# Performance work log

Hardware: AMD Instinct MI355X
Metric: run time of the kernel (lower is better)

The kernel has to match this reference:

```python
import math
import jax, jax.numpy as jnp
import numpy as np

EPS_NORM = 1e-6
EPS_COS = 1e-6


def setup_inputs() -> dict:
    key = jax.random.key(0)
    ks = jax.random.split(key, 6)
    B, C, T, H, W = 2, 768, 8, 24, 24
    d_head = 64
    nh = C // d_head  # 12
    x = jax.random.normal(ks[0], (B, C, T, H, W), jnp.float32)
    pos = jax.random.uniform(ks[1], (B, H, W, 2), jnp.float32)
    cond = jax.random.normal(ks[2], (B, C), jnp.float32)
    # NOTE: original zero-inits norm.linear and out_proj; we use small random
    # weights so the reference exercises the full math path.
    norm_w = jax.random.normal(ks[3], (C, C), jnp.float32) * 0.02
    qkv_w = jax.random.normal(ks[4], (3 * C, C), jnp.float32) * (1.0 / math.sqrt(C))
    scale = jnp.full((nh,), 10.0, jnp.float32)
    out_w = jax.random.normal(ks[5], (C, C), jnp.float32) * 0.02
    # AxialRoPE freqs buffer, exactly as in torch:
    dim = d_head // 2
    n = nh * dim // 4
    lf = np.linspace(math.log(math.pi), math.log(10.0 * math.pi), n + 1)[:-1]
    freqs = jnp.asarray(np.exp(lf).reshape(dim // 4, nh).T, jnp.float32)  # [nh, d_head//8]
    return dict(x=x, pos=pos, cond=cond, norm_w=norm_w, qkv_w=qkv_w,
                scale=scale, out_w=out_w, freqs=freqs)


def reference(x, pos, cond, norm_w, qkv_w, scale, out_w, freqs):
    B, C, T, H, W = x.shape
    nh = freqs.shape[0]
    e = C // nh
    s = H * W
    n = B * T
    skip = x

    # b c t h w -> (b t) h w c
    xr = jnp.transpose(x, (0, 2, 3, 4, 1)).reshape(n, H, W, C)
    # cond: b c -> (b t) c
    condr = jnp.repeat(cond, T, axis=0)

    # AdaRMSNorm
    cs = condr @ norm_w.T + 1.0  # [n, C]
    ms = jnp.mean(xr.astype(jnp.float32) ** 2, axis=-1, keepdims=True)
    xn = (xr * (cs[:, None, None, :] * jax.lax.rsqrt(ms + EPS_NORM))).astype(x.dtype)

    # QKV projection
    qkv = xn @ qkv_w.T  # [n, H, W, 3C]
    qkv = qkv.reshape(n, s, 3, nh, e)
    q = jnp.transpose(qkv[:, :, 0], (0, 2, 1, 3))  # [n, nh, s, e]
    k = jnp.transpose(qkv[:, :, 1], (0, 2, 1, 3))
    v = jnp.transpose(qkv[:, :, 2], (0, 2, 1, 3))

    # cosine-sim QK rescale (per-head learned scale)
    sq = jnp.sqrt(scale)[:, None, None]  # [nh,1,1]
    q = q * (sq * jax.lax.rsqrt(jnp.sum(q ** 2, axis=-1, keepdims=True) + EPS_COS))
    k = k * (sq * jax.lax.rsqrt(jnp.sum(k ** 2, axis=-1, keepdims=True) + EPS_COS))

    # axial RoPE: theta [B, s, nh, 2*dth] -> repeat over T -> [n, nh, s, d]
    posf = pos.reshape(B, s, 2)
    th = posf[:, :, 0, None, None] * freqs  # [B, s, nh, dth]
    tw = posf[:, :, 1, None, None] * freqs
    theta = jnp.concatenate([th, tw], axis=-1)
    theta = jnp.repeat(theta, T, axis=0)
    theta = jnp.transpose(theta, (0, 2, 1, 3))  # [n, nh, s, d]
    cos_t, sin_t = jnp.cos(theta), jnp.sin(theta)
    d = theta.shape[-1]

    def rot(t):
        t1, t2, rest = t[..., :d], t[..., d:2 * d], t[..., 2 * d:]
        return jnp.concatenate([t1 * cos_t - t2 * sin_t,
                                t2 * cos_t + t1 * sin_t, rest], axis=-1)

    q = rot(q)
    k = rot(k)

    # SDPA with scale=1.0
    attn = jax.nn.softmax(jnp.einsum('bhqe,bhke->bhqk', q, k), axis=-1)
    o = jnp.einsum('bhqk,bhke->bhqe', attn, v)  # [n, nh, s, e]

    # n nh (h w) e -> n h w (nh e)
    o = jnp.transpose(o, (0, 2, 1, 3)).reshape(n, H, W, C)
    o = o @ out_w.T
    # (b t) h w c -> b c t h w
    o = o.reshape(B, T, H, W, C).transpose(0, 4, 1, 2, 3)
    return o + skip
```

## Files before the change

### kernel.cpp

```cpp
#include <hip/hip_runtime.h>
#include <hip/hip_bf16.h>

#define CDIM 768
#define NHEAD 12
#define EDIM 64
#define TDIM 8
#define SDIM 576
#define NROW 16
#define MDIM 9216
#define QKVN 2304

typedef __attribute__((ext_vector_type(4))) float f32x4;
typedef __bf16 bf16x8 __attribute__((ext_vector_type(8)));
typedef unsigned short u16;
typedef __attribute__((ext_vector_type(8))) unsigned short u16x8;

__device__ inline float bf2f(u16 u) {
  union { unsigned int i; float f; } x; x.i = ((unsigned int)u) << 16; return x.f;
}
__device__ inline u16 f2bf(float f) {
  union { float f; unsigned int i; } x; x.f = f;
  unsigned int i = x.i;
  return (u16)((i + 0x7FFFu + ((i >> 16) & 1u)) >> 16);
}
__device__ inline unsigned cvt_pk_bf16(float lo, float hi) {
  unsigned r;
  asm("v_cvt_pk_bf16_f32 %0, %1, %2" : "=v"(r) : "v"(lo), "v"(hi));
  return r;
}

__global__ __launch_bounds__(256) void cs_kernel(const float* __restrict__ cond,
                                                 const float* __restrict__ nw,
                                                 float* __restrict__ cs) {
  int idx = blockIdx.x * 256 + threadIdx.x;
  int b = idx / CDIM, c = idx % CDIM;
  const float* cr = cond + (size_t)b * CDIM;
  const float* wr = nw + (size_t)c * CDIM;
  float s = 1.0f;
  for (int j = 0; j < CDIM; j += 4) {
    float4 a = *(const float4*)(cr + j);
    float4 w = *(const float4*)(wr + j);
    s = fmaf(a.x, w.x, s); s = fmaf(a.y, w.y, s);
    s = fmaf(a.z, w.z, s); s = fmaf(a.w, w.w, s);
  }
  cs[idx] = s;
}

__global__ __launch_bounds__(256) void norm_kernel(const float* __restrict__ x,
                                                   const float* __restrict__ cs,
                                                   u16* __restrict__ xn) {
  __shared__ float xs[16][772];
  __shared__ float red[16][17];
  __shared__ float rfac[16];
  int n = blockIdx.y;
  int hw0 = blockIdx.x * 16;
  int b = n >> 3, t = n & 7;
  int tx = threadIdx.x, ty = threadIdx.y;
  const float* xb = x + ((size_t)b * CDIM * TDIM + t) * SDIM;
  float acc = 0.0f;
  for (int c = ty; c < CDIM; c += 16) {
    float v = xb[(size_t)c * (TDIM * SDIM) + hw0 + tx];
    xs[tx][c] = v;
    acc = fmaf(v, v, acc);
  }
  red[ty][tx] = acc;
  __syncthreads();
  if (ty == 0) {
    float s = 0.0f;
    #pragma unroll
    for (int j = 0; j < 16; j++) s += red[j][tx];
    rfac[tx] = rsqrtf(s * (1.0f / (float)CDIM) + 1e-6f);
  }
  __syncthreads();
  const float* csb = cs + (size_t)b * CDIM;
  int flat = ty * 16 + tx;
  #pragma unroll
  for (int i = 0; i < 6; i++) {
    int idx = i * 256 + flat;
    int row = idx / 96;
    int cseg = idx - row * 96;
    int c0 = cseg * 8;
    float rf = rfac[row];
    float4 a0 = *(const float4*)&xs[row][c0];
    float4 a1 = *(const float4*)&xs[row][c0 + 4];
    float4 w0 = *(const float4*)(csb + c0);
    float4 w1 = *(const float4*)(csb + c0 + 4);
    u16x8 ov;
    ov[0] = f2bf(a0.x * w0.x * rf); ov[1] = f2bf(a0.y * w0.y * rf);
    ov[2] = f2bf(a0.z * w0.z * rf); ov[3] = f2bf(a0.w * w0.w * rf);
    ov[4] = f2bf(a1.x * w1.x * rf); ov[5] = f2bf(a1.y * w1.y * rf);
    ov[6] = f2bf(a1.z * w1.z * rf); ov[7] = f2bf(a1.w * w1.w * rf);
    *(u16x8*)(xn + ((size_t)n * SDIM + hw0 + row) * CDIM + c0) = ov;
  }
}

__global__ __launch_bounds__(256) void convert_kernel(const float* __restrict__ src,
                                                      u16* __restrict__ dst, int count4) {
  int i = blockIdx.x * 256 + threadIdx.x;
  if (i < count4) {
    float4 v = *(const float4*)(src + (size_t)i * 4);
    u16* d = dst + (size_t)i * 4;
    d[0] = f2bf(v.x); d[1] = f2bf(v.y); d[2] = f2bf(v.z); d[3] = f2bf(v.w);
  }
}

__device__ __forceinline__ void gemm_bt_lds(const u16* __restrict__ A,
                                            const u16* __restrict__ B,
                                            int K, int m0, int n0, int tid,
                                            u16* ldsA, u16* ldsB,
                                            f32x4 acc[4][4]) {
  int lane = tid & 63;
  int wid = tid >> 6;
  int wm = (wid >> 1) * 64, wn = (wid & 1) * 64;
  int lr = lane & 15, lg = lane >> 4;
  const u16* gA = A + (size_t)(m0 + wid * 32 + (lane >> 3)) * K + (((lane & 7) ^ (lane >> 3)) * 8);
  const u16* gB = B + (size_t)(n0 + wid * 32 + (lane >> 3)) * K + (((lane & 7) ^ (lane >> 3)) * 8);
  u16* dA = ldsA + wid * 2048;
  u16* dB = ldsB + wid * 2048;
  auto STAGE = [&](int buf, int k0) {
    u16* dAb = dA + buf * 8192;
    u16* dBb = dB + buf * 8192;
    #pragma unroll
    for (int is = 0; is < 4; is++) {
      __builtin_amdgcn_global_load_lds(
          (const __attribute__((address_space(1))) unsigned int*)(gA + (size_t)(is * 8) * K + k0),
          (__attribute__((address_space(3))) unsigned int*)(dAb + is * 512),
          16, 0, 0);
      __builtin_amdgcn_global_load_lds(
          (const __attribute__((address_space(1))) unsigned int*)(gB + (size_t)(is * 8) * K + k0),
          (__attribute__((address_space(3))) unsigned int*)(dBb + is * 512),
          16, 0, 0);
    }
  };
  int nt = K >> 6;
  STAGE(0, 0);
  int cur = 0;
  #pragma unroll 1
  for (int t = 0; t < nt; t++) {
    if (t + 1 < nt) {
      STAGE(cur ^ 1, (t + 1) * 64);
      asm volatile("s_waitcnt vmcnt(8)" ::: "memory");
    } else {
      asm volatile("s_waitcnt vmcnt(0)" ::: "memory");
    }
    __builtin_amdgcn_s_barrier();
    __builtin_amdgcn_sched_barrier(0);
    const u16* lA = ldsA + cur * 8192;
    const u16* lB = ldsB + cur * 8192;
    #pragma unroll
    for (int kk = 0; kk < 2; kk++) {
      bf16x8 af[4], bfr[4];
      #pragma unroll
      for (int i = 0; i < 4; i++)
        af[i]  = *(const bf16x8*)&lA[(wm + i * 16 + lr) * 64 + (((lg + 4 * kk) ^ (lr & 7)) * 8)];
      #pragma unroll
      for (int j = 0; j < 4; j++)
        bfr[j] = *(const bf16x8*)&lB[(wn + j * 16 + lr) * 64 + (((lg + 4 * kk) ^ (lr & 7)) * 8)];
      #pragma unroll
      for (int i = 0; i < 4; i++)
        #pragma unroll
        for (int j = 0; j < 4; j++)
          acc[i][j] = __builtin_amdgcn_mfma_f32_16x16x32_bf16(af[i], bfr[j], acc[i][j], 0, 0, 0);
    }
    __builtin_amdgcn_sched_barrier(0);
    __builtin_amdgcn_s_barrier();
    __builtin_amdgcn_sched_barrier(0);
    cur ^= 1;
  }
}

__device__ __forceinline__ void swz_tile(int L, int& m0, int& n0) {
  int xcd = L & 7, loc = L >> 3;
  int nblk = loc / 9, mloc = loc - nblk * 9;
  m0 = (xcd * 9 + mloc) * 128;
  n0 = nblk * 128;
}

__global__ __launch_bounds__(256) void gemm_qkv(const u16* __restrict__ xn,
                                                const u16* __restrict__ wq,
                                                const float* __restrict__ pos,
                                                const float* __restrict__ freqs,
                                                const float* __restrict__ scale,
                                                u16* __restrict__ q,
                                                u16* __restrict__ k,
                                                u16* __restrict__ vt) {
  __shared__ u16 smem[32768];
  u16* ldsA = smem;
  u16* ldsB = smem + 16384;
  f32x4 acc[4][4] = {};
  int tid = threadIdx.x;
  int m0, n0;
  swz_tile(blockIdx.x, m0, n0);
  gemm_bt_lds(xn, wq, CDIM, m0, n0, tid, ldsA, ldsB, acc);
  int lane = tid & 63, wid = tid >> 6;
  int wm = (wid >> 1) * 64, wn = (wid & 1) * 64;
  int lr = lane & 15, rb = (lane >> 4) * 4;
  int part = n0 / CDIM;
  int hbase = (n0 - part * CDIM) >> 6;
  u16* T = smem;
  if (part < 2) {
    int h = hbase + (wn >> 6);
    float fr = freqs[h * 8 + (lr & 7)];
    float sq = sqrtf(scale[h]) * (part == 0 ? 1.44269504f : 1.0f);
    #pragma unroll
    for (int i = 0; i < 4; i++)
      #pragma unroll
      for (int r = 0; r < 4; r++) {
        int m = m0 + wm + i * 16 + rb + r;
        int nidx = m / SDIM, sp = m - nidx * SDIM;
        int b = nidx >> 3;
        float2 pp = *(const float2*)&pos[((size_t)b * SDIM + sp) * 2];
        float th = (lr < 8 ? pp.x : pp.y) * fr;
        float sth, cth;
        __sincosf(th, &sth, &cth);
        float v0 = acc[i][0][r];
        float v1 = acc[i][1][r];
        float v2 = acc[i][2][r];
        float v3 = acc[i][3][r];
        float ss = v0 * v0 + v1 * v1 + v2 * v2 + v3 * v3;
        ss += __shfl_xor(ss, 1); ss += __shfl_xor(ss, 2);
        ss += __shfl_xor(ss, 4); ss += __shfl_xor(ss, 8);
        float rs = sq * rsqrtf(ss + 1e-6f);
        v0 *= rs; v1 *= rs; v2 *= rs; v3 *= rs;
        float o0 = v0 * cth - v1 * sth;
        float o1 = v1 * cth + v0 * sth;
        u16* trow = T + (size_t)(wm + i * 16 + rb + r) * 136 + wn + lr;
        trow[0]  = f2bf(o0); trow[16] = f2bf(o1);
        trow[32] = f2bf(v2); trow[48] = f2bf(v3);
      }
    __syncthreads();
    u16* dst = (part == 0) ? q : k;
    #pragma unroll
    for (int c = 0; c < 8; c++) {
      int chunk = c * 256 + tid;
      int ml = chunk >> 4, sub = chunk & 15;
      int m = m0 + ml;
      int nidx = m / SDIM, sp = m - nidx * SDIM;
      int hl = sub >> 3, e0 = (sub & 7) * 8;
      u16x8 v = *(const u16x8*)&T[(size_t)ml * 136 + sub * 8];
      *(u16x8*)(dst + ((size_t)(nidx * NHEAD + hbase + hl) * SDIM + sp) * EDIM + e0) = v;
    }
  } else {
    #pragma unroll
    for (int i = 0; i < 4; i++)
      #pragma unroll
      for (int j = 0; j < 4; j++)
        #pragma unroll
        for (int r = 0; r < 4; r++)
          T[(size_t)(wn + j * 16 + lr) * 136 + (wm + i * 16 + rb + r)] = f2bf(acc[i][j][r]);
    __syncthreads();
    #pragma unroll
    for (int c = 0; c < 8; c++) {
      int chunk = c * 256 + tid;
      int nl = chunk >> 4, sub = chunk & 15;
      int hl = nl >> 6, e = nl & 63;
      int m = m0 + sub * 8;
      int nidx = m / SDIM, hw = m - nidx * SDIM;
      u16x8 v = *(const u16x8*)&T[(size_t)nl * 136 + sub * 8];
      *(u16x8*)(vt + ((size_t)(nidx * NHEAD + hbase + hl) * EDIM + e) * SDIM + hw) = v;
    }
  }
}

__global__ __launch_bounds__(256, 2) void attn_mfma(const u16* __restrict__ q,
                                                    const u16* __restrict__ k,
                                                    const u16* __restrict__ vt,
                                                    u16* __restrict__ o) {
  __shared__ u16 kbuf[2][4096];
  __shared__ u16 vbuf[2][4096];
  __shared__ u16 p_lds[4][48][72];
  int L = blockIdx.x;
  int cid = (L & 7) * 72 + (L >> 3);
  int nh_ = cid / 3;
  int qt = cid - nh_ * 3;
  int n = nh_ / NHEAD, h = nh_ - n * NHEAD;
  int tid = threadIdx.x;
  int wid = tid >> 6, lane = tid & 63;
  int lr = lane & 15, lg = lane >> 4;
  int qbase = qt * 192 + wid * 48;

  const u16* qp = q + ((size_t)nh_ * SDIM + qbase) * EDIM;
  bf16x8 qa[3][2];
  #pragma unroll
  for (int f = 0; f < 3; f++) {
    qa[f][0] = *(const bf16x8*)(qp + (size_t)(f * 16 + lr) * EDIM + lg * 8);
    qa[f][1] = *(const bf16x8*)(qp + (size_t)(f * 16 + lr) * EDIM + 32 + lg * 8);
  }
  const u16* kb = k + (size_t)nh_ * SDIM * EDIM;
  const u16* vb = vt + (size_t)nh_ * EDIM * SDIM;

  int srow = wid * 16 + (lane >> 3);
  int schunk = (lane & 7) ^ (lane >> 3);
  auto STAGE = [&](int buf, int s0) {
    #pragma unroll
    for (int is = 0; is < 2; is++) {
      int row = srow + is * 8;
      __builtin_amdgcn_global_load_lds(
          (const __attribute__((address_space(1))) unsigned int*)(kb + (size_t)(s0 + row) * EDIM + schunk * 8),
          (__attribute__((address_space(3))) unsigned int*)(&kbuf[buf][(size_t)(wid * 16 + is * 8 + (lane >> 3)) * 64 + (lane & 7) * 8]),
          16, 0, 0);
      __builtin_amdgcn_global_load_lds(
          (const __attribute__((address_space(1))) unsigned int*)(vb + (size_t)row * SDIM + s0 + schunk * 8),
          (__attribute__((address_space(3))) unsigned int*)(&vbuf[buf][(size_t)(wid * 16 + is * 8 + (lane >> 3)) * 64 + (lane & 7) * 8]),
          16, 0, 0);
    }
  };

  float psum[3] = {0.0f, 0.0f, 0.0f};
  f32x4 oacc[3][4] = {};

  STAGE(0, 0);
  int cur = 0;
  #pragma unroll 1
  for (int kt = 0; kt < 9; kt++) {
    if (kt < 8) {
      STAGE(cur ^ 1, (kt + 1) * 64);
      asm volatile("s_waitcnt vmcnt(4)" ::: "memory");
    } else {
      asm volatile("s_waitcnt vmcnt(0)" ::: "memory");
    }
    __builtin_amdgcn_s_barrier();
    __builtin_amdgcn_sched_barrier(0);
    const u16* kl = kbuf[cur];
    const u16* vl = vbuf[cur];
    bf16x8 kf[4][2];
    #pragma unroll
    for (int j = 0; j < 4; j++) {
      kf[j][0] = *(const bf16x8*)&kl[(j * 16 + lr) * 64 + ((lg       ^ (lr & 7)) * 8)];
      kf[j][1] = *(const bf16x8*)&kl[(j * 16 + lr) * 64 + (((lg + 4) ^ (lr & 7)) * 8)];
    }
    bf16x8 vf[2][4];
    #pragma unroll
    for (int ks = 0; ks < 2; ks++)
      #pragma unroll
      for (int et = 0; et < 4; et++)
        vf[ks][et] = *(const bf16x8*)&vl[(et * 16 + lr) * 64 + (((ks * 4 + lg) ^ (lr & 7)) * 8)];
    #pragma unroll
    for (int f = 0; f < 3; f++) {
      f32x4 sfr[4] = {};
      #pragma unroll
      for (int j = 0; j < 4; j++) {
        sfr[j] = __builtin_amdgcn_mfma_f32_16x16x32_bf16(kf[j][0], qa[f][0], sfr[j], 0, 0, 0);
        sfr[j] = __builtin_amdgcn_mfma_f32_16x16x32_bf16(kf[j][1], qa[f][1], sfr[j], 0, 0, 0);
      }
      float fs = 0.0f;
      #pragma unroll
      for (int j = 0; j < 4; j++) {
        float p0 = exp2f(sfr[j][0]);
        float p1 = exp2f(sfr[j][1]);
        float p2 = exp2f(sfr[j][2]);
        float p3 = exp2f(sfr[j][3]);
        unsigned w0 = cvt_pk_bf16(p0, p1);
        unsigned w1 = cvt_pk_bf16(p2, p3);
        *(unsigned*)&p_lds[wid][f * 16 + lr][j * 16 + lg * 4]     = w0;
        *(unsigned*)&p_lds[wid][f * 16 + lr][j * 16 + lg * 4 + 2] = w1;
        fs += (p0 + p1) + (p2 + p3);
      }
      psum[f] += fs;
    }
    #pragma unroll
    for (int f = 0; f < 3; f++)
      #pragma unroll
      for (int ks = 0; ks < 2; ks++) {
        bf16x8 pa = *(const bf16x8*)&p_lds[wid][f * 16 + lr][ks * 32 + lg * 8];
        #pragma unroll
        for (int et = 0; et < 4; et++)
          oacc[f][et] = __builtin_amdgcn_mfma_f32_16x16x32_bf16(pa, vf[ks][et], oacc[f][et], 0, 0, 0);
      }
    __builtin_amdgcn_sched_barrier(0);
    __builtin_amdgcn_s_barrier();
    __builtin_amdgcn_sched_barrier(0);
    cur ^= 1;
  }
  u16* ob = o + ((size_t)n * SDIM + qbase) * CDIM + h * EDIM;
  #pragma unroll
  for (int f = 0; f < 3; f++) {
    float s = psum[f];
    s += __shfl_xor(s, 16);
    s += __shfl_xor(s, 32);
    float inv = 1.0f / s;
    #pragma unroll
    for (int r = 0; r < 4; r++) {
      float invr = __shfl(inv, lg * 4 + r);
      #pragma unroll
      for (int et = 0; et < 4; et++)
        ob[(size_t)(f * 16 + lg * 4 + r) * CDIM + et * 16 + lr] = f2bf(oacc[f][et][r] * invr);
    }
  }
}

__global__ __launch_bounds__(256) void gemm_proj(const u16* __restrict__ o,
                                                 const u16* __restrict__ wo,
                                                 const float* __restrict__ x,
                                                 float* __restrict__ out) {
  __shared__ __align__(16) char smem[128 * 132 * 4];
  u16* ldsA = (u16*)smem;
  u16* ldsB = (u16*)smem + 16384;
  f32x4 acc[4][4] = {};
  int tid = threadIdx.x;
  int m0, n0;
  swz_tile(blockIdx.x, m0, n0);
  gemm_bt_lds(o, wo, CDIM, m0, n0, tid, ldsA, ldsB, acc);
  int lane = tid & 63, wid = tid >> 6;
  int wm = (wid >> 1) * 64, wn = (wid & 1) * 64;
  int lr = lane & 15, rb = (lane >> 4) * 4;
  float* T = (float*)smem;
  #pragma unroll
  for (int i = 0; i < 4; i++)
    #pragma unroll
    for (int j = 0; j < 4; j++)
      #pragma unroll
      for (int r = 0; r < 4; r++)
        T[(size_t)(wn + j * 16 + lr) * 132 + (wm + i * 16 + rb + r)] = acc[i][j][r];
  __syncthreads();
  #pragma unroll
  for (int c = 0; c < 16; c++) {
    int chunk = c * 256 + tid;
    int nl = chunk >> 5, sub = chunk & 31;
    int m = m0 + sub * 4;
    int nidx = m / SDIM, hw = m - nidx * SDIM;
    int b = nidx >> 3, t = nidx & 7;
    int jj = n0 + nl;
    size_t oi = ((size_t)(b * CDIM + jj) * TDIM + t) * SDIM + hw;
    float4 xv = *(const float4*)&x[oi];
    float4 tv = *(const float4*)&T[(size_t)nl * 132 + sub * 4];
    float4 ov;
    ov.x = tv.x + xv.x; ov.y = tv.y + xv.y;
    ov.z = tv.z + xv.z; ov.w = tv.w + xv.w;
    *(float4*)&out[oi] = ov;
  }
}

extern "C" void kernel_launch(void* const* d_in, const int* in_sizes, int n_in,
                              void* d_out, int out_size, void* d_ws, size_t ws_size,
                              hipStream_t stream) {
  const float* x      = (const float*)d_in[0];
  const float* pos    = (const float*)d_in[1];
  const float* cond   = (const float*)d_in[2];
  const float* norm_w = (const float*)d_in[3];
  const float* qkv_w  = (const float*)d_in[4];
  const float* scale  = (const float*)d_in[5];
  const float* out_w  = (const float*)d_in[6];
  const float* freqs  = (const float*)d_in[7];
  float* out = (float*)d_out;

  char* ws = (char*)d_ws;
  size_t off = 0;
  auto alloc = [&](size_t bytes) -> char* {
    char* p = ws + off;
    off = (off + bytes + 255) & ~(size_t)255;
    return p;
  };
  float* cs  = (float*)alloc(2 * CDIM * sizeof(float));
  u16* wq    = (u16*)alloc((size_t)QKVN * CDIM * 2);
  u16* wo    = (u16*)alloc((size_t)CDIM * CDIM * 2);
  u16* xn    = (u16*)alloc((size_t)MDIM * CDIM * 2);
  u16* qb    = (u16*)alloc((size_t)MDIM * CDIM * 2);
  u16* kb    = (u16*)alloc((size_t)MDIM * CDIM * 2);
  u16* vt    = (u16*)alloc((size_t)MDIM * CDIM * 2);
  u16* ob    = (u16*)alloc((size_t)MDIM * CDIM * 2);

  convert_kernel<<<dim3((QKVN * CDIM / 4 + 255) / 256), dim3(256), 0, stream>>>(qkv_w, wq, QKVN * CDIM / 4);
  convert_kernel<<<dim3((CDIM * CDIM / 4 + 255) / 256), dim3(256), 0, stream>>>(out_w, wo, CDIM * CDIM / 4);
  cs_kernel<<<dim3(6), dim3(256), 0, stream>>>(cond, norm_w, cs);
  norm_kernel<<<dim3(SDIM / 16, NROW), dim3(16, 16), 0, stream>>>(x, cs, xn);
  gemm_qkv<<<dim3(8 * 9 * (QKVN / 128)), dim3(256), 0, stream>>>(xn, wq, pos, freqs, scale, qb, kb, vt);
  attn_mfma<<<dim3(576), dim3(256), 0, stream>>>(qb, kb, vt, ob);
  gemm_proj<<<dim3(8 * 9 * (CDIM / 128)), dim3(256), 0, stream>>>(ob, wo, x, out);
}
```

Before: 167.0 us.

## Fuse prep kernels, precompute RoPE trig table, triple-buffer attention K/V with setprio

The two weight conversions, the cond projection and a new RoPE cos/sin table are merged into one prep launch. The QKV GEMM epilogue now reads the precomputed trig values instead of computing sincos inline. The attention kernel moves from double to triple buffering of K/V tiles, issues each prefetch after the barrier, drops the trailing barrier, and raises wave priority around the MFMA sections. These aim to cut launch overhead, epilogue math and load stalls, at the cost of more LDS per block (possibly lower occupancy) and an extra global table read.

```diff
diff --git a/kernel.cpp b/kernel.cpp
--- a/kernel.cpp
+++ b/kernel.cpp
@@ -29,21 +29,52 @@
   return r;
 }
 
-__global__ __launch_bounds__(256) void cs_kernel(const float* __restrict__ cond,
-                                                 const float* __restrict__ nw,
-                                                 float* __restrict__ cs) {
-  int idx = blockIdx.x * 256 + threadIdx.x;
-  int b = idx / CDIM, c = idx % CDIM;
-  const float* cr = cond + (size_t)b * CDIM;
-  const float* wr = nw + (size_t)c * CDIM;
-  float s = 1.0f;
-  for (int j = 0; j < CDIM; j += 4) {
-    float4 a = *(const float4*)(cr + j);
-    float4 w = *(const float4*)(wr + j);
-    s = fmaf(a.x, w.x, s); s = fmaf(a.y, w.y, s);
-    s = fmaf(a.z, w.z, s); s = fmaf(a.w, w.w, s);
-  }
-  cs[idx] = s;
+__global__ __launch_bounds__(256) void prep_kernel(const float* __restrict__ qkv_w,
+                                                   u16* __restrict__ wq,
+                                                   const float* __restrict__ out_w,
+                                                   u16* __restrict__ wo,
+                                                   const float* __restrict__ cond,
+                                                   const float* __restrict__ nw,
+                                                   float* __restrict__ cs,
+                                                   const float* __restrict__ pos,
+                                                   const float* __restrict__ freqs,
+                                                   float2* __restrict__ trig) {
+  int bid = blockIdx.x;
+  int tid = threadIdx.x;
+  if (bid < 1728) {
+    int i = bid * 256 + tid;
+    float4 v = *(const float4*)(qkv_w + (size_t)i * 4);
+    u16* d = wq + (size_t)i * 4;
+    d[0] = f2bf(v.x); d[1] = f2bf(v.y); d[2] = f2bf(v.z); d[3] = f2bf(v.w);
+  } else if (bid < 2304) {
+    int i = (bid - 1728) * 256 + tid;
+    float4 v = *(const float4*)(out_w + (size_t)i * 4);
+    u16* d = wo + (size_t)i * 4;
+    d[0] = f2bf(v.x); d[1] = f2bf(v.y); d[2] = f2bf(v.z); d[3] = f2bf(v.w);
+  } else if (bid < 2310) {
+    int idx = (bid - 2304) * 256 + tid;
+    int b = idx / CDIM, c = idx - b * CDIM;
+    const float* cr = cond + (size_t)b * CDIM;
+    const float* wr = nw + (size_t)c * CDIM;
+    float s = 1.0f;
+    for (int j = 0; j < CDIM; j += 4) {
+      float4 a = *(const float4*)(cr + j);
+      float4 w = *(const float4*)(wr + j);
+      s = fmaf(a.x, w.x, s); s = fmaf(a.y, w.y, s);
+      s = fmaf(a.z, w.z, s); s = fmaf(a.w, w.w, s);
+    }
+    cs[idx] = s;
+  } else {
+    int idx = (bid - 2310) * 256 + tid;
+    int j = idx & 15;
+    int h = (idx >> 4) % NHEAD;
+    int bs = idx / (16 * NHEAD);
+    float p = pos[(size_t)bs * 2 + (j >> 3)];
+    float th = p * freqs[h * 8 + (j & 7)];
+    float sn, cn;
+    __sincosf(th, &sn, &cn);
+    trig[idx] = make_float2(cn, sn);
+  }
 }
 
 __global__ __launch_bounds__(256) void norm_kernel(const float* __restrict__ x,
@@ -94,16 +125,6 @@
   }
 }
 
-__global__ __launch_bounds__(256) void convert_kernel(const float* __restrict__ src,
-                                                      u16* __restrict__ dst, int count4) {
-  int i = blockIdx.x * 256 + threadIdx.x;
-  if (i < count4) {
-    float4 v = *(const float4*)(src + (size_t)i * 4);
-    u16* d = dst + (size_t)i * 4;
-    d[0] = f2bf(v.x); d[1] = f2bf(v.y); d[2] = f2bf(v.z); d[3] = f2bf(v.w);
-  }
-}
-
 __device__ __forceinline__ void gemm_bt_lds(const u16* __restrict__ A,
                                             const u16* __restrict__ B,
                                             int K, int m0, int n0, int tid,
@@ -178,8 +199,7 @@
 
 __global__ __launch_bounds__(256) void gemm_qkv(const u16* __restrict__ xn,
                                                 const u16* __restrict__ wq,
-                                                const float* __restrict__ pos,
-                                                const float* __restrict__ freqs,
+                                                const float2* __restrict__ trig,
                                                 const float* __restrict__ scale,
                                                 u16* __restrict__ q,
                                                 u16* __restrict__ k,
@@ -200,7 +220,6 @@
   u16* T = smem;
   if (part < 2) {
     int h = hbase + (wn >> 6);
-    float fr = freqs[h * 8 + (lr & 7)];
     float sq = sqrtf(scale[h]) * (part == 0 ? 1.44269504f : 1.0f);
     #pragma unroll
     for (int i = 0; i < 4; i++)
@@ -209,10 +228,7 @@
         int m = m0 + wm + i * 16 + rb + r;
         int nidx = m / SDIM, sp = m - nidx * SDIM;
         int b = nidx >> 3;
-        float2 pp = *(const float2*)&pos[((size_t)b * SDIM + sp) * 2];
-        float th = (lr < 8 ? pp.x : pp.y) * fr;
-        float sth, cth;
-        __sincosf(th, &sth, &cth);
+        float2 cssn = trig[(((size_t)b * SDIM + sp) * NHEAD + h) * 16 + lr];
         float v0 = acc[i][0][r];
         float v1 = acc[i][1][r];
         float v2 = acc[i][2][r];
@@ -222,8 +238,8 @@
         ss += __shfl_xor(ss, 4); ss += __shfl_xor(ss, 8);
         float rs = sq * rsqrtf(ss + 1e-6f);
         v0 *= rs; v1 *= rs; v2 *= rs; v3 *= rs;
-        float o0 = v0 * cth - v1 * sth;
-        float o1 = v1 * cth + v0 * sth;
+        float o0 = v0 * cssn.x - v1 * cssn.y;
+        float o1 = v1 * cssn.x + v0 * cssn.y;
         u16* trow = T + (size_t)(wm + i * 16 + rb + r) * 136 + wn + lr;
         trow[0]  = f2bf(o0); trow[16] = f2bf(o1);
         trow[32] = f2bf(v2); trow[48] = f2bf(v3);
@@ -266,8 +282,8 @@
                                                     const u16* __restrict__ k,
                                                     const u16* __restrict__ vt,
                                                     u16* __restrict__ o) {
-  __shared__ u16 kbuf[2][4096];
-  __shared__ u16 vbuf[2][4096];
+  __shared__ u16 kbuf[3][4096];
+  __shared__ u16 vbuf[3][4096];
   __shared__ u16 p_lds[4][48][72];
   int L = blockIdx.x;
   int cid = (L & 7) * 72 + (L >> 3);
@@ -310,19 +326,19 @@
   f32x4 oacc[3][4] = {};
 
   STAGE(0, 0);
-  int cur = 0;
+  STAGE(1, 64);
   #pragma unroll 1
   for (int kt = 0; kt < 9; kt++) {
     if (kt < 8) {
-      STAGE(cur ^ 1, (kt + 1) * 64);
       asm volatile("s_waitcnt vmcnt(4)" ::: "memory");
     } else {
       asm volatile("s_waitcnt vmcnt(0)" ::: "memory");
     }
     __builtin_amdgcn_s_barrier();
     __builtin_amdgcn_sched_barrier(0);
-    const u16* kl = kbuf[cur];
-    const u16* vl = vbuf[cur];
+    if (kt < 7) STAGE((kt + 2) % 3, (kt + 2) * 64);
+    const u16* kl = kbuf[kt % 3];
+    const u16* vl = vbuf[kt % 3];
     bf16x8 kf[4][2];
     #pragma unroll
     for (int j = 0; j < 4; j++) {
@@ -338,11 +354,13 @@
     #pragma unroll
     for (int f = 0; f < 3; f++) {
       f32x4 sfr[4] = {};
+      __builtin_amdgcn_s_setprio(1);
       #pragma unroll
       for (int j = 0; j < 4; j++) {
         sfr[j] = __builtin_amdgcn_mfma_f32_16x16x32_bf16(kf[j][0], qa[f][0], sfr[j], 0, 0, 0);
         sfr[j] = __builtin_amdgcn_mfma_f32_16x16x32_bf16(kf[j][1], qa[f][1], sfr[j], 0, 0, 0);
       }
+      __builtin_amdgcn_s_setprio(0);
       float fs = 0.0f;
       #pragma unroll
       for (int j = 0; j < 4; j++) {
@@ -358,6 +376,7 @@
       }
       psum[f] += fs;
     }
+    __builtin_amdgcn_s_setprio(1);
     #pragma unroll
     for (int f = 0; f < 3; f++)
       #pragma unroll
@@ -367,10 +386,8 @@
         for (int et = 0; et < 4; et++)
           oacc[f][et] = __builtin_amdgcn_mfma_f32_16x16x32_bf16(pa, vf[ks][et], oacc[f][et], 0, 0, 0);
       }
+    __builtin_amdgcn_s_setprio(0);
     __builtin_amdgcn_sched_barrier(0);
-    __builtin_amdgcn_s_barrier();
-    __builtin_amdgcn_sched_barrier(0);
-    cur ^= 1;
   }
   u16* ob = o + ((size_t)n * SDIM + qbase) * CDIM + h * EDIM;
   #pragma unroll
@@ -451,20 +468,20 @@
     off = (off + bytes + 255) & ~(size_t)255;
     return p;
   };
-  float* cs  = (float*)alloc(2 * CDIM * sizeof(float));
-  u16* wq    = (u16*)alloc((size_t)QKVN * CDIM * 2);
-  u16* wo    = (u16*)alloc((size_t)CDIM * CDIM * 2);
-  u16* xn    = (u16*)alloc((size_t)MDIM * CDIM * 2);
-  u16* qb    = (u16*)alloc((size_t)MDIM * CDIM * 2);
-  u16* kb    = (u16*)alloc((size_t)MDIM * CDIM * 2);
-  u16* vt    = (u16*)alloc((size_t)MDIM * CDIM * 2);
-  u16* ob    = (u16*)alloc((size_t)MDIM * CDIM * 2);
-
-  convert_kernel<<<dim3((QKVN * CDIM / 4 + 255) / 256), dim3(256), 0, stream>>>(qkv_w, wq, QKVN * CDIM / 4);
-  convert_kernel<<<dim3((CDIM * CDIM / 4 + 255) / 256), dim3(256), 0, stream>>>(out_w, wo, CDIM * CDIM / 4);
-  cs_kernel<<<dim3(6), dim3(256), 0, stream>>>(cond, norm_w, cs);
+  float* cs   = (float*)alloc(2 * CDIM * sizeof(float));
+  u16* wq     = (u16*)alloc((size_t)QKVN * CDIM * 2);
+  u16* wo     = (u16*)alloc((size_t)CDIM * CDIM * 2);
+  u16* xn     = (u16*)alloc((size_t)MDIM * CDIM * 2);
+  u16* qb     = (u16*)alloc((size_t)MDIM * CDIM * 2);
+  u16* kb     = (u16*)alloc((size_t)MDIM * CDIM * 2);
+  u16* vt     = (u16*)alloc((size_t)MDIM * CDIM * 2);
+  u16* ob     = (u16*)alloc((size_t)MDIM * CDIM * 2);
+  float2* trg = (float2*)alloc((size_t)2 * SDIM * NHEAD * 16 * sizeof(float2));
+
+  prep_kernel<<<dim3(3174), dim3(256), 0, stream>>>(qkv_w, wq, out_w, wo,
+                                                    cond, norm_w, cs, pos, freqs, trg);
   norm_kernel<<<dim3(SDIM / 16, NROW), dim3(16, 16), 0, stream>>>(x, cs, xn);
-  gemm_qkv<<<dim3(8 * 9 * (QKVN / 128)), dim3(256), 0, stream>>>(xn, wq, pos, freqs, scale, qb, kb, vt);
+  gemm_qkv<<<dim3(8 * 9 * (QKVN / 128)), dim3(256), 0, stream>>>(xn, wq, trg, scale, qb, kb, vt);
   attn_mfma<<<dim3(576), dim3(256), 0, stream>>>(qb, kb, vt, ob);
   gemm_proj<<<dim3(8 * 9 * (CDIM / 128)), dim3(256), 0, stream>>>(ob, wo, x, out);
 }
```

New measurement: 163.9 us. No clear change (-1.9%).
